# Performance work log

Hardware: AMD Instinct MI355X
Metric: run time of the kernel (lower is better)

The kernel has to match this reference:

```python
import jax, jax.numpy as jnp
import numpy as np

SHIFTS = [1, 3, 5, 7]
C = 16  # in_channels // 4
# -1 neighbor offsets for tmp1..tmp8 (dy, dx) in units of the dilation
OFFSETS = [(-1, -1), (-1, 0), (-1, 1), (0, 1), (1, 1), (1, 0), (1, -1), (0, -1)]


def setup_inputs() -> dict:
    key = jax.random.key(0)
    ks = jax.random.split(key, 32)
    d = {}
    d['cen'] = jax.random.normal(ks[0], (8, 64, 256, 256), jnp.float32)
    d['mas'] = jax.random.normal(ks[1], (8, 1, 256, 256), jnp.float32)
    d['in_conv_w'] = jax.random.normal(ks[2], (16, 64), jnp.float32) * 0.1
    d['in_conv_b'] = jax.random.normal(ks[3], (16,), jnp.float32) * 0.1
    for i, s in enumerate(SHIFTS):
        d[f'dw_w{s}'] = jax.random.normal(ks[4 + 2 * i], (16, 1, s, s), jnp.float32) * 0.1
        d[f'dw_b{s}'] = jax.random.normal(ks[5 + 2 * i], (16,), jnp.float32) * 0.1
    d['l1_w'] = jax.random.normal(ks[12], (4, 16, 4), jnp.float32) * 0.1
    d['l1_b'] = jax.random.normal(ks[13], (4, 16), jnp.float32) * 0.1
    d['l2_w'] = jax.random.normal(ks[14], (4, 16, 8), jnp.float32) * 0.1
    d['l2_b'] = jax.random.normal(ks[15], (4, 16), jnp.float32) * 0.1
    d['base_w'] = jax.random.normal(ks[16], (16, 4), jnp.float32) * 0.1
    d['bn_scale'] = jnp.ones((16,), jnp.float32)
    d['bn_bias'] = jnp.zeros((16,), jnp.float32)
    d['final_w'] = jax.random.normal(ks[17], (1, 16), jnp.float32) * 0.1
    d['final_b'] = jax.random.normal(ks[18], (1,), jnp.float32) * 0.1
    return d


def _dw_conv(x, w, b, pad):
    # depthwise conv, groups == channels
    y = jax.lax.conv_general_dilated(
        x, w, window_strides=(1, 1), padding=[(pad, pad), (pad, pad)],
        dimension_numbers=('NCHW', 'OIHW', 'NCHW'), feature_group_count=x.shape[1])
    return y + b[None, :, None, None]


def _shifted(x, dy, dx, d):
    # zero-padded shift: out(y,x) = in(y+dy, x+dx)
    H, W = x.shape[2], x.shape[3]
    p = jnp.pad(x, ((0, 0), (0, 0), (d, d), (d, d)))
    return p[:, :, d + dy:d + dy + H, d + dx:d + dx + W]


def _circ_shift(x, dw_w, dw_b, w1, b1, w2, b2, shift):
    x = _dw_conv(x, dw_w, dw_b, shift // 2)
    # tmp_k = x - x shifted by the k-th neighbor offset (dilation = shift)
    T = [x - _shifted(x, dy * shift, dx * shift, shift) for dy, dx in OFFSETS]
    # paired sums: S[k] = tmp_{k+1} + tmp_{k+5} (S repeats with period 4)
    S = [T[k] + T[k + 4] for k in range(4)]
    outs = []
    for k in range(8):  # fixed small structural loop
        feats = jnp.stack([S[(k + 1) % 4], S[(k + 3) % 4], S[(k + 2) % 4],
                           2.0 * T[(k + 4) % 8]], axis=2)  # (B,C,4,H,W)
        # grouped 1x1 conv (groups=C, 4C->C) == per-channel contraction over feature axis
        o = jnp.einsum('bcfhw,cf->bchw', feats, w1) + b1[None, :, None, None]
        outs.append(o * T[k])
    O = jnp.sort(jnp.stack(outs, axis=2), axis=2)  # (B,C,8,H,W) sorted over branch axis
    return jnp.einsum('bcfhw,cf->bchw', O, w2) + b2[None, :, None, None]


def reference(cen, mas, in_conv_w, in_conv_b, dw_w1, dw_b1, dw_w3, dw_b3,
              dw_w5, dw_b5, dw_w7, dw_b7, l1_w, l1_b, l2_w, l2_b,
              base_w, bn_scale, bn_bias, final_w, final_b):
    # in_conv: 1x1, in_channels -> C
    x = jnp.einsum('bihw,oi->bohw', cen, in_conv_w) + in_conv_b[None, :, None, None]
    dws = [(dw_w1, dw_b1), (dw_w3, dw_b3), (dw_w5, dw_b5), (dw_w7, dw_b7)]
    branches = [
        _circ_shift(x, dws[i][0], dws[i][1], l1_w[i], l1_b[i], l2_w[i], l2_b[i], SHIFTS[i])
        for i in range(len(SHIFTS))
    ]
    A = jnp.sort(jnp.stack(branches, axis=2), axis=2)  # (B,C,4,H,W)
    # out_conv: grouped 1x1 BaseConv (conv no-bias + BN(affine) + SiLU), then 1x1 -> 1, sigmoid
    y = jnp.einsum('bcfhw,cf->bchw', A, base_w)
    y = jax.nn.silu(y * bn_scale[None, :, None, None] + bn_bias[None, :, None, None])
    y = jnp.einsum('bchw,oc->bohw', y, final_w) + final_b[None, :, None, None]
    return jax.nn.sigmoid(y)
```

## Files before the change

### kernel.cpp

```cpp
#include <hip/hip_runtime.h>
#include <hip/hip_fp16.h>
#include <math.h>

#define HW 65536

typedef float v2f __attribute__((ext_vector_type(2), aligned(8)));
typedef _Float16 h2 __attribute__((ext_vector_type(2)));

__device__ __forceinline__ h2 uh(unsigned u) { return __builtin_bit_cast(h2, u); }
__device__ __forceinline__ unsigned hu(h2 v) { return __builtin_bit_cast(unsigned, v); }

#define CEH(a, b) { h2 _t = __builtin_elementwise_min(a, b); \
                    b = __builtin_elementwise_max(a, b); a = _t; }

__device__ __forceinline__ void sort8_h2(h2* v) {
    CEH(v[0], v[1]); CEH(v[2], v[3]); CEH(v[4], v[5]); CEH(v[6], v[7]);
    CEH(v[0], v[2]); CEH(v[1], v[3]); CEH(v[4], v[6]); CEH(v[5], v[7]);
    CEH(v[1], v[2]); CEH(v[5], v[6]); CEH(v[0], v[4]); CEH(v[3], v[7]);
    CEH(v[1], v[5]); CEH(v[2], v[6]);
    CEH(v[1], v[4]); CEH(v[3], v[6]);
    CEH(v[2], v[4]); CEH(v[3], v[5]);
    CEH(v[3], v[4]);
}
__device__ __forceinline__ void sort4_h2(h2* v) {
    CEH(v[0], v[1]); CEH(v[2], v[3]); CEH(v[0], v[2]); CEH(v[1], v[3]); CEH(v[1], v[2]);
}

__global__ __launch_bounds__(256) void k_pack(const float* __restrict__ l1w,
                                              const float* __restrict__ l1b,
                                              const float* __restrict__ l2w,
                                              const float* __restrict__ l2b,
                                              const float* __restrict__ bw,
                                              const float* __restrict__ dw_w1,
                                              const float* __restrict__ dw_b1,
                                              const float* __restrict__ dw_w3,
                                              const float* __restrict__ dw_b3,
                                              const float* __restrict__ dw_w5,
                                              const float* __restrict__ dw_b5,
                                              const float* __restrict__ dw_w7,
                                              const float* __restrict__ dw_b7,
                                              unsigned* __restrict__ wtab) {
    for (int t = threadIdx.x; t < 3584; t += 256) {
        float v = 0.f;
        if (t < 1024) {
            int c = t >> 6, i = (t >> 4) & 3, j = t & 15;
            if (j < 3)        v = l1w[i * 64 + c * 4 + j];
            else if (j == 3)  v = 2.f * l1w[i * 64 + c * 4 + 3];
            else if (j == 4)  v = l1b[i * 16 + c];
            else if (j < 13)  v = l2w[i * 128 + c * 8 + (j - 5)];
            else if (j == 13) v = l2b[i * 16 + c];
        } else if (t < 1088) {
            v = bw[t - 1024];
        } else if (t >= 2048) {
            int c = (t - 2048) / 96, j = (t - 2048) - c * 96;
            if (j < 49)       v = dw_w7[c * 49 + j];
            else if (j < 74)  v = dw_w5[c * 25 + (j - 49)];
            else if (j < 83)  v = dw_w3[c * 9 + (j - 74)];
            else if (j == 83) v = dw_w1[c];
            else if (j == 84) v = dw_b1[c];
            else if (j == 85) v = dw_b3[c];
            else if (j == 86) v = dw_b5[c];
            else if (j == 87) v = dw_b7[c];
        }
        unsigned hs = (unsigned)__half_as_ushort(__float2half(v));
        wtab[t] = hs * 0x10001u;
    }
}

__global__ __launch_bounds__(256, 4) void k_inconv(const float* __restrict__ cen,
                                                   const float* __restrict__ w,
                                                   const float* __restrict__ bias,
                                                   __half* __restrict__ xh) {
    __shared__ float wl[1040];
    int tid = threadIdx.x;
    for (int t = tid; t < 1024; t += 256) wl[t] = w[(t & 15) * 64 + (t >> 4)];
    if (tid < 16) wl[1024 + tid] = bias[tid];
    __syncthreads();

    int pr = blockIdx.x * 256 + tid;
    int b_ = pr >> 15;
    int hw = (pr & 32767) * 2;
    const float* src = cen + (size_t)(b_ * 64) * HW + hw;

    v2f acc[16];
#pragma unroll
    for (int o = 0; o < 16; o++) { float bv = wl[1024 + o]; v2f t = {bv, bv}; acc[o] = t; }

#pragma unroll 8
    for (int i = 0; i < 64; i++) {
        v2f xv = *(const v2f*)(src + (size_t)i * HW);
        const float4* wq = (const float4*)&wl[i * 16];
#pragma unroll
        for (int g = 0; g < 4; g++) {
            float4 f = wq[g];
            acc[g * 4 + 0] += xv * f.x;
            acc[g * 4 + 1] += xv * f.y;
            acc[g * 4 + 2] += xv * f.z;
            acc[g * 4 + 3] += xv * f.w;
        }
    }
    __half* dst = xh + (size_t)(b_ * 16) * HW + hw;
#pragma unroll
    for (int o = 0; o < 16; o++)
        *(__half2*)(dst + (size_t)o * HW) = __floats2half2_rn(acc[o].x, acc[o].y);
}

#define LXS 43
#define CTS 40
#define CTP (78 * CTS)
__global__ __launch_bounds__(1024, 4) void k_fused(const __half* __restrict__ xh,
    const unsigned* __restrict__ wtab,
    const float* __restrict__ bns, const float* __restrict__ bnb,
    __half* __restrict__ y16) {

    const int by  = blockIdx.y;
    const int c   = by & 15;
    const int ty0 = (blockIdx.x >> 2) * 64;
    const int tx0 = (blockIdx.x & 3) * 64;
    const int tid = threadIdx.x;

    __shared__ unsigned lxh[84 * LXS];
    __shared__ unsigned convt[4 * CTP];

    {
        const unsigned* xp32 = (const unsigned*)(xh + (size_t)by * HW);
        for (int t = tid; t < 84 * 42; t += 1024) {
            int r = t / 42, j = t - r * 42;
            int gy = ty0 - 10 + r, gp = tx0 - 10 + 2 * j;
            unsigned v = 0;
            if ((unsigned)gy < 256u && (unsigned)gp < 256u)
                v = xp32[(gy << 7) + (gp >> 1)];
            lxh[r * LXS + j] = v;
        }
    }
    __syncthreads();

    {
        const unsigned* dwc = wtab + 2048 + c * 96;
        for (int u = tid; u < 78 * 39; u += 1024) {
            int row = u / 39;
            int d0  = u - row * 39;
            h2 acc7 = {0, 0}, acc5 = {0, 0}, acc3 = {0, 0}, acc1 = {0, 0};
#pragma unroll
            for (int a = 0; a < 7; a++) {
                const unsigned* rp = lxh + (row + a) * LXS + d0;
                unsigned q0 = rp[0], q1 = rp[1], q2 = rp[2], q3 = rp[3];
                unsigned p1u = (q0 >> 16) | (q1 << 16);
                unsigned p3u = (q1 >> 16) | (q2 << 16);
                unsigned p5u = (q2 >> 16) | (q3 << 16);
                h2 P[7] = {uh(q0), uh(p1u), uh(q1), uh(p3u),
                           uh(q2), uh(p5u), uh(q3)};
#pragma unroll
                for (int b = 0; b < 7; b++)
                    acc7 = P[b] * uh(dwc[a * 7 + b]) + acc7;
                if (a >= 1 && a <= 5) {
#pragma unroll
                    for (int b = 0; b < 5; b++)
                        acc5 = P[1 + b] * uh(dwc[49 + (a - 1) * 5 + b]) + acc5;
                }
                if (a >= 2 && a <= 4) {
#pragma unroll
                    for (int b = 0; b < 3; b++)
                        acc3 = P[2 + b] * uh(dwc[74 + (a - 2) * 3 + b]) + acc3;
                }
                if (a == 3)
                    acc1 = P[3] * uh(dwc[83]);
            }
            int iy = ty0 - 7 + row, ix = tx0 - 7 + 2 * d0;
            bool rin = (unsigned)iy < 256u;
            unsigned msk = (rin && (unsigned)ix < 256u ? 0x0000FFFFu : 0u)
                         | (rin && (unsigned)(ix + 1) < 256u ? 0xFFFF0000u : 0u);
            int o = row * CTS + d0;
            convt[o]           = hu(acc1 + uh(dwc[84])) & msk;
            convt[o + CTP]     = hu(acc3 + uh(dwc[85])) & msk;
            convt[o + 2 * CTP] = hu(acc5 + uh(dwc[86])) & msk;
            convt[o + 3 * CTP] = hu(acc7 + uh(dwc[87])) & msk;
        }
    }
    __syncthreads();

    const int py  = tid >> 5;
    const int pxp = tid & 31;

#pragma unroll
    for (int rr = 0; rr < 2; rr++) {
        const int R = py + (rr << 5);

        h2 bh[4];
#pragma unroll
        for (int i = 0; i < 4; i++) {
            const int s = 1 + 2 * i;
            const unsigned* pl = convt + i * CTP;
            const int q    = pxp + (7 - s) / 2;
            const int topb = (R + 7 - s) * CTS + q;
            const int midb = (R + 7) * CTS + q;
            const int botb = (R + 7 + s) * CTS + q;

            unsigned tt[8], tm[8], tb[8];
#pragma unroll
            for (int k = 0; k <= s; k++) {
                tt[k] = pl[topb + k];
                tm[k] = pl[midb + k];
                tb[k] = pl[botb + k];
            }
            const int m = s >> 1;
            h2 n0  = uh(tt[0]);
            h2 n1  = uh((tt[m] >> 16) | (tt[m + 1] << 16));
            h2 n2  = uh(tt[s]);
            h2 n7  = uh(tm[0]);
            h2 ctr = uh((tm[m] >> 16) | (tm[m + 1] << 16));
            h2 n3  = uh(tm[s]);
            h2 n6  = uh(tb[0]);
            h2 n5  = uh((tb[m] >> 16) | (tb[m + 1] << 16));
            h2 n4  = uh(tb[s]);

            h2 T[8];
            T[0] = ctr - n0; T[1] = ctr - n1; T[2] = ctr - n2; T[3] = ctr - n3;
            T[4] = ctr - n4; T[5] = ctr - n5; T[6] = ctr - n6; T[7] = ctr - n7;
            h2 S[4];
#pragma unroll
            for (int k = 0; k < 4; k++) S[k] = T[k] + T[k + 4];

            const unsigned* wt = wtab + ((c << 2) + i) * 16;
            h2 w10 = uh(wt[0]), w11 = uh(wt[1]), w12 = uh(wt[2]);
            h2 w13x2 = uh(wt[3]), bb1 = uh(wt[4]);

            h2 R4[4];
#pragma unroll
            for (int mm = 0; mm < 4; mm++) {
                h2 r = S[(mm + 2) & 3] * w12 + bb1;
                r = S[(mm + 3) & 3] * w11 + r;
                r = S[(mm + 1) & 3] * w10 + r;
                R4[mm] = r;
            }
            h2 h8[8];
#pragma unroll
            for (int k = 0; k < 8; k++)
                h8[k] = (T[(k + 4) & 7] * w13x2 + R4[k & 3]) * T[k];
            sort8_h2(h8);

            h2 acc = uh(wt[13]);
#pragma unroll
            for (int k = 0; k < 8; k++) acc += h8[k] * uh(wt[5 + k]);
            bh[i] = acc;
        }
        sort4_h2(bh);
        h2 yv = bh[0] * uh(wtab[1024 + (c << 2)]);
#pragma unroll
        for (int k = 1; k < 4; k++) yv = bh[k] * uh(wtab[1024 + (c << 2) + k]) + yv;

        const float bsc = bns[c], bbi = bnb[c];
        float zx = fmaf((float)yv.x, bsc, bbi);
        float zy = fmaf((float)yv.y, bsc, bbi);
        float sx = zx / (1.f + __expf(-zx));
        float sy = zy / (1.f + __expf(-zy));
        *(__half2*)&y16[(size_t)by * HW + (ty0 + R) * 256 + tx0 + 2 * pxp] =
            __floats2half2_rn(sx, sy);
    }
}

__global__ __launch_bounds__(256) void k_final(const __half* __restrict__ y16,
                                               const float* __restrict__ fw,
                                               const float* __restrict__ fb,
                                               float* __restrict__ out) {
    long t  = (long)blockIdx.x * 256 + threadIdx.x;
    long p0 = t * 2;
    int  b  = (int)(p0 >> 16);
    int  hw = (int)(p0 & 65535);

    float accx = fb[0], accy = fb[0];
#pragma unroll
    for (int cc = 0; cc < 16; cc++) {
        __half2 h = *(const __half2*)(y16 + (size_t)(b * 16 + cc) * HW + hw);
        float2 v = __half22float2(h);
        float wv = fw[cc];
        accx = fmaf(v.x, wv, accx);
        accy = fmaf(v.y, wv, accy);
    }
    float2 r;
    r.x = 1.f / (1.f + __expf(-accx));
    r.y = 1.f / (1.f + __expf(-accy));
    *(float2*)(out + p0) = r;
}

extern "C" void kernel_launch(void* const* d_in, const int* in_sizes, int n_in,
                              void* d_out, int out_size, void* d_ws, size_t ws_size,
                              hipStream_t stream) {
    (void)in_sizes; (void)n_in; (void)out_size; (void)ws_size;
    const float* cen   = (const float*)d_in[0];
    const float* in_w  = (const float*)d_in[2];
    const float* in_b  = (const float*)d_in[3];
    const float* dw_w1 = (const float*)d_in[4];
    const float* dw_b1 = (const float*)d_in[5];
    const float* dw_w3 = (const float*)d_in[6];
    const float* dw_b3 = (const float*)d_in[7];
    const float* dw_w5 = (const float*)d_in[8];
    const float* dw_b5 = (const float*)d_in[9];
    const float* dw_w7 = (const float*)d_in[10];
    const float* dw_b7 = (const float*)d_in[11];
    const float* l1w   = (const float*)d_in[12];
    const float* l1b   = (const float*)d_in[13];
    const float* l2w   = (const float*)d_in[14];
    const float* l2b   = (const float*)d_in[15];
    const float* bw    = (const float*)d_in[16];
    const float* bns   = (const float*)d_in[17];
    const float* bnb   = (const float*)d_in[18];
    const float* fw    = (const float*)d_in[19];
    const float* fb    = (const float*)d_in[20];

    __half*   xh   = (__half*)d_ws;
    unsigned* wtab = (unsigned*)((char*)d_ws + (size_t)16777216);
    __half*   y16  = (__half*)((char*)d_ws + (size_t)16777216 + 16384);
    float*    out  = (float*)d_out;

    k_pack<<<1, 256, 0, stream>>>(l1w, l1b, l2w, l2b, bw,
                                  dw_w1, dw_b1, dw_w3, dw_b3,
                                  dw_w5, dw_b5, dw_w7, dw_b7, wtab);
    k_inconv<<<1024, 256, 0, stream>>>(cen, in_w, in_b, xh);
    k_fused<<<dim3(16, 128), 1024, 0, stream>>>(xh, wtab, bns, bnb, y16);
    k_final<<<1024, 256, 0, stream>>>(y16, fw, fb, out);
}
```

Before: 344.7 us.

## Process two half2 pixel pairs per thread with 64-bit LDS accesses in fused kernel

```diff
diff --git a/kernel.cpp b/kernel.cpp
--- a/kernel.cpp
+++ b/kernel.cpp
@@ -9,6 +9,9 @@
 
 __device__ __forceinline__ h2 uh(unsigned u) { return __builtin_bit_cast(h2, u); }
 __device__ __forceinline__ unsigned hu(h2 v) { return __builtin_bit_cast(unsigned, v); }
+__device__ __forceinline__ unsigned algn(unsigned lo, unsigned hi) {
+    return (lo >> 16) | (hi << 16);
+}
 
 #define CEH(a, b) { h2 _t = __builtin_elementwise_min(a, b); \
                     b = __builtin_elementwise_max(a, b); a = _t; }
@@ -105,10 +108,82 @@
         *(__half2*)(dst + (size_t)o * HW) = __floats2half2_rn(acc[o].x, acc[o].y);
 }
 
-#define LXS 43
-#define CTS 40
+#define LXS 44
+#define CTS 42
 #define CTP (78 * CTS)
-__global__ __launch_bounds__(1024, 4) void k_fused(const __half* __restrict__ xh,
+
+template<int S, int PAD>
+__device__ __forceinline__ void branch_pair(const unsigned* pl, int R, int g,
+                                            const unsigned* wt, h2* outA, h2* outB) {
+    const int D = 2 * g + (7 - S) / 2 + PAD;
+    const int L = (S + 3) / 2;
+    const unsigned* pt = pl + (R + 7 - S) * CTS + D;
+    const unsigned* pm = pl + (R + 7) * CTS + D;
+    const unsigned* pb = pl + (R + 7 + S) * CTS + D;
+    unsigned ut[2 * L], um[2 * L], ub[2 * L];
+#pragma unroll
+    for (int k = 0; k < L; k++) {
+        *(uint2*)&ut[2 * k] = *(const uint2*)(pt + 2 * k);
+        *(uint2*)&um[2 * k] = *(const uint2*)(pm + 2 * k);
+        *(uint2*)&ub[2 * k] = *(const uint2*)(pb + 2 * k);
+    }
+#pragma unroll
+    for (int dw = 0; dw < 2; dw++) {
+        h2 n0 = uh(ut[dw]);
+        h2 n1 = uh(algn(ut[(S - 1) / 2 + dw], ut[(S + 1) / 2 + dw]));
+        h2 n2 = uh(ut[S + dw]);
+        h2 n7 = uh(um[dw]);
+        h2 ct = uh(algn(um[(S - 1) / 2 + dw], um[(S + 1) / 2 + dw]));
+        h2 n3 = uh(um[S + dw]);
+        h2 n6 = uh(ub[dw]);
+        h2 n5 = uh(algn(ub[(S - 1) / 2 + dw], ub[(S + 1) / 2 + dw]));
+        h2 n4 = uh(ub[S + dw]);
+
+        h2 T[8];
+        T[0] = ct - n0; T[1] = ct - n1; T[2] = ct - n2; T[3] = ct - n3;
+        T[4] = ct - n4; T[5] = ct - n5; T[6] = ct - n6; T[7] = ct - n7;
+        h2 Sm[4];
+#pragma unroll
+        for (int k = 0; k < 4; k++) Sm[k] = T[k] + T[k + 4];
+
+        h2 w10 = uh(wt[0]), w11 = uh(wt[1]), w12 = uh(wt[2]);
+        h2 w13x2 = uh(wt[3]), bb1 = uh(wt[4]);
+
+        h2 R4[4];
+#pragma unroll
+        for (int mm = 0; mm < 4; mm++) {
+            h2 r = Sm[(mm + 2) & 3] * w12 + bb1;
+            r = Sm[(mm + 3) & 3] * w11 + r;
+            r = Sm[(mm + 1) & 3] * w10 + r;
+            R4[mm] = r;
+        }
+        h2 h8[8];
+#pragma unroll
+        for (int k = 0; k < 8; k++)
+            h8[k] = (T[(k + 4) & 7] * w13x2 + R4[k & 3]) * T[k];
+        sort8_h2(h8);
+
+        h2 acc = uh(wt[13]);
+#pragma unroll
+        for (int k = 0; k < 8; k++) acc += h8[k] * uh(wt[5 + k]);
+        if (dw == 0) *outA = acc; else *outB = acc;
+    }
+}
+
+__device__ __forceinline__ unsigned tail_px(h2* bh, const unsigned* __restrict__ wtab,
+                                            int c, float bsc, float bbi) {
+    sort4_h2(bh);
+    h2 yv = bh[0] * uh(wtab[1024 + (c << 2)]);
+#pragma unroll
+    for (int k = 1; k < 4; k++) yv = bh[k] * uh(wtab[1024 + (c << 2) + k]) + yv;
+    float zx = fmaf((float)yv.x, bsc, bbi);
+    float zy = fmaf((float)yv.y, bsc, bbi);
+    float sx = zx / (1.f + __expf(-zx));
+    float sy = zy / (1.f + __expf(-zy));
+    return __builtin_bit_cast(unsigned, __floats2half2_rn(sx, sy));
+}
+
+__global__ __launch_bounds__(1024, 8) void k_fused(const __half* __restrict__ xh,
     const unsigned* __restrict__ wtab,
     const float* __restrict__ bns, const float* __restrict__ bnb,
     __half* __restrict__ y16) {
@@ -124,139 +199,96 @@
 
     {
         const unsigned* xp32 = (const unsigned*)(xh + (size_t)by * HW);
-        for (int t = tid; t < 84 * 42; t += 1024) {
-            int r = t / 42, j = t - r * 42;
-            int gy = ty0 - 10 + r, gp = tx0 - 10 + 2 * j;
-            unsigned v = 0;
-            if ((unsigned)gy < 256u && (unsigned)gp < 256u)
-                v = xp32[(gy << 7) + (gp >> 1)];
-            lxh[r * LXS + j] = v;
+        for (int t = tid; t < 84 * 21; t += 1024) {
+            int r = t / 21, j = t - r * 21;
+            int gy = ty0 - 10 + r;
+            int gp = tx0 - 10 + 4 * j;
+            unsigned v0 = 0, v1 = 0;
+            if ((unsigned)gy < 256u) {
+                const unsigned* rp = xp32 + (gy << 7);
+                if ((unsigned)gp < 256u)       v0 = rp[gp >> 1];
+                if ((unsigned)(gp + 2) < 256u) v1 = rp[(gp >> 1) + 1];
+            }
+            uint2 st = {v0, v1};
+            *(uint2*)&lxh[r * LXS + 2 * j] = st;
         }
     }
     __syncthreads();
 
     {
         const unsigned* dwc = wtab + 2048 + c * 96;
-        for (int u = tid; u < 78 * 39; u += 1024) {
-            int row = u / 39;
-            int d0  = u - row * 39;
-            h2 acc7 = {0, 0}, acc5 = {0, 0}, acc3 = {0, 0}, acc1 = {0, 0};
+        for (int u = tid; u < 78 * 20; u += 1024) {
+            int row = u / 20;
+            int g   = u - row * 20;
+            h2 a7A = {0, 0}, a7B = {0, 0}, a5A = {0, 0}, a5B = {0, 0};
+            h2 a3A = {0, 0}, a3B = {0, 0}, a1A = {0, 0}, a1B = {0, 0};
 #pragma unroll
             for (int a = 0; a < 7; a++) {
-                const unsigned* rp = lxh + (row + a) * LXS + d0;
-                unsigned q0 = rp[0], q1 = rp[1], q2 = rp[2], q3 = rp[3];
-                unsigned p1u = (q0 >> 16) | (q1 << 16);
-                unsigned p3u = (q1 >> 16) | (q2 << 16);
-                unsigned p5u = (q2 >> 16) | (q3 << 16);
-                h2 P[7] = {uh(q0), uh(p1u), uh(q1), uh(p3u),
-                           uh(q2), uh(p5u), uh(q3)};
-#pragma unroll
-                for (int b = 0; b < 7; b++)
-                    acc7 = P[b] * uh(dwc[a * 7 + b]) + acc7;
+                const unsigned* rp = lxh + (row + a) * LXS + 2 * g;
+                uint2 w0 = *(const uint2*)rp;
+                uint2 w1 = *(const uint2*)(rp + 2);
+                uint2 w2 = *(const uint2*)(rp + 4);
+                unsigned u0 = w0.x, u1 = w0.y, u2 = w1.x, u3 = w1.y, u4 = w2.x;
+                h2 E[9] = {uh(u0), uh(algn(u0, u1)), uh(u1), uh(algn(u1, u2)),
+                           uh(u2), uh(algn(u2, u3)), uh(u3), uh(algn(u3, u4)), uh(u4)};
+#pragma unroll
+                for (int b = 0; b < 7; b++) {
+                    h2 wv = uh(dwc[a * 7 + b]);
+                    a7A = E[b] * wv + a7A;  a7B = E[b + 2] * wv + a7B;
+                }
                 if (a >= 1 && a <= 5) {
 #pragma unroll
-                    for (int b = 0; b < 5; b++)
-                        acc5 = P[1 + b] * uh(dwc[49 + (a - 1) * 5 + b]) + acc5;
+                    for (int b = 0; b < 5; b++) {
+                        h2 wv = uh(dwc[49 + (a - 1) * 5 + b]);
+                        a5A = E[b + 1] * wv + a5A;  a5B = E[b + 3] * wv + a5B;
+                    }
                 }
                 if (a >= 2 && a <= 4) {
 #pragma unroll
-                    for (int b = 0; b < 3; b++)
-                        acc3 = P[2 + b] * uh(dwc[74 + (a - 2) * 3 + b]) + acc3;
+                    for (int b = 0; b < 3; b++) {
+                        h2 wv = uh(dwc[74 + (a - 2) * 3 + b]);
+                        a3A = E[b + 2] * wv + a3A;  a3B = E[b + 4] * wv + a3B;
+                    }
                 }
-                if (a == 3)
-                    acc1 = P[3] * uh(dwc[83]);
+                if (a == 3) {
+                    h2 wv = uh(dwc[83]);
+                    a1A = E[3] * wv;  a1B = E[5] * wv;
+                }
             }
-            int iy = ty0 - 7 + row, ix = tx0 - 7 + 2 * d0;
+            int iy = ty0 - 7 + row;
             bool rin = (unsigned)iy < 256u;
-            unsigned msk = (rin && (unsigned)ix < 256u ? 0x0000FFFFu : 0u)
-                         | (rin && (unsigned)(ix + 1) < 256u ? 0xFFFF0000u : 0u);
-            int o = row * CTS + d0;
-            convt[o]           = hu(acc1 + uh(dwc[84])) & msk;
-            convt[o + CTP]     = hu(acc3 + uh(dwc[85])) & msk;
-            convt[o + 2 * CTP] = hu(acc5 + uh(dwc[86])) & msk;
-            convt[o + 3 * CTP] = hu(acc7 + uh(dwc[87])) & msk;
+            int ix0 = tx0 - 7 + 4 * g;
+            unsigned mA = (rin && (unsigned)ix0 < 256u ? 0x0000FFFFu : 0u)
+                        | (rin && (unsigned)(ix0 + 1) < 256u ? 0xFFFF0000u : 0u);
+            unsigned mB = (rin && (unsigned)(ix0 + 2) < 256u ? 0x0000FFFFu : 0u)
+                        | (rin && (unsigned)(ix0 + 3) < 256u ? 0xFFFF0000u : 0u);
+            int o = row * CTS + 2 * g;
+            uint2 s3 = {hu(a3A + uh(dwc[85])) & mA, hu(a3B + uh(dwc[85])) & mB};
+            uint2 s7 = {hu(a7A + uh(dwc[87])) & mA, hu(a7B + uh(dwc[87])) & mB};
+            *(uint2*)&convt[CTP + o]     = s3;
+            *(uint2*)&convt[3 * CTP + o] = s7;
+            convt[o + 1]                 = hu(a1A + uh(dwc[84])) & mA;
+            convt[o + 2]                 = hu(a1B + uh(dwc[84])) & mB;
+            convt[2 * CTP + o + 1]       = hu(a5A + uh(dwc[86])) & mA;
+            convt[2 * CTP + o + 2]       = hu(a5B + uh(dwc[86])) & mB;
         }
     }
     __syncthreads();
 
-    const int py  = tid >> 5;
-    const int pxp = tid & 31;
-
-#pragma unroll
-    for (int rr = 0; rr < 2; rr++) {
-        const int R = py + (rr << 5);
-
-        h2 bh[4];
-#pragma unroll
-        for (int i = 0; i < 4; i++) {
-            const int s = 1 + 2 * i;
-            const unsigned* pl = convt + i * CTP;
-            const int q    = pxp + (7 - s) / 2;
-            const int topb = (R + 7 - s) * CTS + q;
-            const int midb = (R + 7) * CTS + q;
-            const int botb = (R + 7 + s) * CTS + q;
-
-            unsigned tt[8], tm[8], tb[8];
-#pragma unroll
-            for (int k = 0; k <= s; k++) {
-                tt[k] = pl[topb + k];
-                tm[k] = pl[midb + k];
-                tb[k] = pl[botb + k];
-            }
-            const int m = s >> 1;
-            h2 n0  = uh(tt[0]);
-            h2 n1  = uh((tt[m] >> 16) | (tt[m + 1] << 16));
-            h2 n2  = uh(tt[s]);
-            h2 n7  = uh(tm[0]);
-            h2 ctr = uh((tm[m] >> 16) | (tm[m + 1] << 16));
-            h2 n3  = uh(tm[s]);
-            h2 n6  = uh(tb[0]);
-            h2 n5  = uh((tb[m] >> 16) | (tb[m + 1] << 16));
-            h2 n4  = uh(tb[s]);
-
-            h2 T[8];
-            T[0] = ctr - n0; T[1] = ctr - n1; T[2] = ctr - n2; T[3] = ctr - n3;
-            T[4] = ctr - n4; T[5] = ctr - n5; T[6] = ctr - n6; T[7] = ctr - n7;
-            h2 S[4];
-#pragma unroll
-            for (int k = 0; k < 4; k++) S[k] = T[k] + T[k + 4];
-
-            const unsigned* wt = wtab + ((c << 2) + i) * 16;
-            h2 w10 = uh(wt[0]), w11 = uh(wt[1]), w12 = uh(wt[2]);
-            h2 w13x2 = uh(wt[3]), bb1 = uh(wt[4]);
-
-            h2 R4[4];
-#pragma unroll
-            for (int mm = 0; mm < 4; mm++) {
-                h2 r = S[(mm + 2) & 3] * w12 + bb1;
-                r = S[(mm + 3) & 3] * w11 + r;
-                r = S[(mm + 1) & 3] * w10 + r;
-                R4[mm] = r;
-            }
-            h2 h8[8];
-#pragma unroll
-            for (int k = 0; k < 8; k++)
-                h8[k] = (T[(k + 4) & 7] * w13x2 + R4[k & 3]) * T[k];
-            sort8_h2(h8);
-
-            h2 acc = uh(wt[13]);
-#pragma unroll
-            for (int k = 0; k < 8; k++) acc += h8[k] * uh(wt[5 + k]);
-            bh[i] = acc;
-        }
-        sort4_h2(bh);
-        h2 yv = bh[0] * uh(wtab[1024 + (c << 2)]);
-#pragma unroll
-        for (int k = 1; k < 4; k++) yv = bh[k] * uh(wtab[1024 + (c << 2) + k]) + yv;
-
-        const float bsc = bns[c], bbi = bnb[c];
-        float zx = fmaf((float)yv.x, bsc, bbi);
-        float zy = fmaf((float)yv.y, bsc, bbi);
-        float sx = zx / (1.f + __expf(-zx));
-        float sy = zy / (1.f + __expf(-zy));
-        *(__half2*)&y16[(size_t)by * HW + (ty0 + R) * 256 + tx0 + 2 * pxp] =
-            __floats2half2_rn(sx, sy);
-    }
+    const int R = tid >> 4;
+    const int g = tid & 15;
+
+    h2 bhA[4], bhB[4];
+    branch_pair<1, 1>(convt,           R, g, wtab + ((c << 2) + 0) * 16, &bhA[0], &bhB[0]);
+    branch_pair<3, 0>(convt + CTP,     R, g, wtab + ((c << 2) + 1) * 16, &bhA[1], &bhB[1]);
+    branch_pair<5, 1>(convt + 2 * CTP, R, g, wtab + ((c << 2) + 2) * 16, &bhA[2], &bhB[2]);
+    branch_pair<7, 0>(convt + 3 * CTP, R, g, wtab + ((c << 2) + 3) * 16, &bhA[3], &bhB[3]);
+
+    const float bsc = bns[c], bbi = bnb[c];
+    unsigned r0 = tail_px(bhA, wtab, c, bsc, bbi);
+    unsigned r1 = tail_px(bhB, wtab, c, bsc, bbi);
+    uint2 st = {r0, r1};
+    *(uint2*)&y16[(size_t)by * HW + (ty0 + R) * 256 + tx0 + 4 * g] = st;
 }
 
 __global__ __launch_bounds__(256) void k_final(const __half* __restrict__ y16,
```

Result: faster. 333.1 us (-3.4%).
